# Kernel tuning notes

Measured on AMD Instinct MI355X. Metric: run time of the kernel, lower is better.

The kernel has to match this reference:

```python
import jax, jax.numpy as jnp
import numpy as np

B, N, D, H = 4, 256, 32, 512

def setup_inputs() -> dict:
    key = jax.random.key(0)
    ks = jax.random.split(key, 6)
    z = jax.random.normal(ks[0], (B, N, D), dtype=jnp.float32)
    motif_mask = (jax.random.uniform(ks[1], (B, N)) > 0.5).astype(jnp.float32)
    residue_mask = jnp.ones((B, N), dtype=jnp.float32)
    # Linear weights stored as (in, out); scaled like torch default init
    W1 = jax.random.normal(ks[2], (D * D, H), dtype=jnp.float32) / np.sqrt(D * D)
    b1 = jnp.zeros((H,), dtype=jnp.float32)
    W2 = jax.random.normal(ks[3], (H, H // 2), dtype=jnp.float32) / np.sqrt(H)
    b2 = jnp.zeros((H // 2,), dtype=jnp.float32)
    W3 = jax.random.normal(ks[4], (H // 2, 1), dtype=jnp.float32) / np.sqrt(H // 2)
    b3 = jnp.zeros((1,), dtype=jnp.float32)
    return {"z": z, "motif_mask": motif_mask, "residue_mask": residue_mask,
            "W1": W1, "b1": b1, "W2": W2, "b2": b2, "W3": W3, "b3": b3}

def reference(z, motif_mask, residue_mask, W1, b1, W2, b2, W3, b3):
    # kron[b,i,j, a*D+c] = z[b,i,a] * z[b,j,c]; first Linear on kron is the
    # bilinear form z_i^T W1_h z_j -- compute via two matmuls, never
    # materializing the (B,N,N,D^2) tensor.
    d = z.shape[-1]
    W1r = W1.reshape(d, d, -1)                      # (D, D, H); axis0 = z_i dim, axis1 = z_j dim
    tmp = jnp.einsum('bia,ach->bihc', z, W1r)        # (B, N, H, D)
    h1 = jax.nn.relu(jnp.einsum('bihc,bjc->bijh', tmp, z) + b1)  # (B, N, N, H)
    h2 = jax.nn.relu(jnp.einsum('bijh,hk->bijk', h1, W2) + b2)   # (B, N, N, H/2)
    contact_logits = (jnp.einsum('bijk,ko->bijo', h2, W3) + b3)[..., 0]  # (B, N, N)
    outer_mask = motif_mask[:, None, :] * motif_mask[:, :, None]
    contact_logits = contact_logits * outer_mask
    contact_map = jax.nn.sigmoid(contact_logits)
    return (contact_map, contact_logits)
```

## Files before the change

### kernel.cpp

```cpp
#include <hip/hip_runtime.h>
#include <hip/hip_bf16.h>
#include <cstdint>
#include <cstddef>

#define NB 4
#define NN 256
#define DD 32
#define HH 512

typedef __attribute__((ext_vector_type(8))) short short8;
typedef __attribute__((ext_vector_type(4))) float f32x4;
typedef __attribute__((ext_vector_type(16))) float f32x16;

static __device__ __forceinline__ unsigned cvtpk(float a, float b) {
  unsigned r;
  asm("v_cvt_pk_bf16_f32 %0, %1, %2" : "=v"(r) : "v"(a), "v"(b));
  return r;
}
static __device__ __forceinline__ unsigned short f2bf1(float a) {
  return (unsigned short)(cvtpk(a, 0.f) & 0xffffu);
}

static __device__ __forceinline__ short8 pack8(float4 a0, float4 a1) {
  union { unsigned u[4]; short8 s; } r;
  r.u[0] = cvtpk(a0.x, a0.y); r.u[1] = cvtpk(a0.z, a0.w);
  r.u[2] = cvtpk(a1.x, a1.y); r.u[3] = cvtpk(a1.z, a1.w);
  return r.s;
}

__global__ __launch_bounds__(256) void prep(const float* __restrict__ z,
                                            const float* __restrict__ W1,
                                            const float* __restrict__ W2,
                                            const float* __restrict__ motif,
                                            unsigned short* __restrict__ W2F,
                                            unsigned short* __restrict__ Tall,
                                            int* __restrict__ jlist,
                                            int* __restrict__ mlist,
                                            int* __restrict__ jcnt) {
  const int blk = blockIdx.x;
  const int tid = threadIdx.x;
  if (blk < 512) {
    __shared__ unsigned short w1s[16384];
    const int nblk = blk >> 4, mgrp = blk & 15;
    const int bibase = mgrp * 64;

    #pragma unroll
    for (int r = 0; r < 16; ++r) {
      int task = r * 256 + tid;
      int row = task >> 2;
      int hq = task & 3;
      float4 v = *(const float4*)(W1 + (size_t)row * 512 + nblk * 16 + hq * 4);
      int a = row >> 5, c = row & 31;
      int quad = a >> 3, e = a & 7;
      float hv[4] = {v.x, v.y, v.z, v.w};
      #pragma unroll
      for (int vv = 0; vv < 4; ++vv) {
        int hl = hq * 4 + vv;
        int nl = hl * 32 + c;
        int w2 = nl >> 7, r7 = nl & 127;
        int l16 = r7 >> 3, nt = r7 & 7;
        w1s[((w2 * 8 + nt) * 64 + quad * 16 + l16) * 8 + e] = f2bf1(hv[vv]);
      }
    }
    __syncthreads();

    const int w2 = tid >> 6, lane = tid & 63;
    const int quad = lane >> 4, l16 = lane & 15;

    short8 bfr[8];
    #pragma unroll
    for (int nt = 0; nt < 8; ++nt)
      bfr[nt] = *(const short8*)&w1s[((w2 * 8 + nt) * 64 + lane) * 8];

    const int ncol = nblk * 512 + w2 * 128 + l16 * 8;
    #pragma unroll
    for (int mtg = 0; mtg < 2; ++mtg) {
      short8 afr[2];
      #pragma unroll
      for (int mi = 0; mi < 2; ++mi) {
        const float* zr = z + (size_t)(bibase + (mtg * 2 + mi) * 16 + l16) * 32 + quad * 8;
        float4 a0 = *(const float4*)(zr);
        float4 a1 = *(const float4*)(zr + 4);
        afr[mi] = pack8(a0, a1);
      }
      f32x4 d[2][8];
      #pragma unroll
      for (int mi = 0; mi < 2; ++mi)
        #pragma unroll
        for (int nt = 0; nt < 8; ++nt)
          d[mi][nt] = __builtin_amdgcn_mfma_f32_16x16x32_bf16(
              afr[mi], bfr[nt], (f32x4){0.f, 0.f, 0.f, 0.f}, 0, 0, 0);
      #pragma unroll
      for (int mi = 0; mi < 2; ++mi)
        #pragma unroll
        for (int r = 0; r < 4; ++r) {
          size_t rowoff = (size_t)(bibase + (mtg * 2 + mi) * 16 + quad * 4 + r) * 16384;
          uint4 p;
          p.x = cvtpk(d[mi][0][r], d[mi][1][r]);
          p.y = cvtpk(d[mi][2][r], d[mi][3][r]);
          p.z = cvtpk(d[mi][4][r], d[mi][5][r]);
          p.w = cvtpk(d[mi][6][r], d[mi][7][r]);
          *(uint4*)&Tall[rowoff + ncol] = p;
        }
    }
  } else if (blk < 576) {
    int f8 = (blk - 512) * 256 + tid;
    int lane = f8 & 63;
    int nt = (f8 >> 6) & 1, s = (f8 >> 7) & 3, hc = (f8 >> 9) & 7, w = (f8 >> 12) & 3;
    int k2 = w * 64 + nt * 32 + (lane & 31);
    int hb = hc * 64 + s * 16 + (lane >> 5) * 8;
    float v[8];
    #pragma unroll
    for (int e = 0; e < 8; ++e) v[e] = W2[(hb + e) * 256 + k2];
    uint4 p;
    p.x = cvtpk(v[0], v[1]); p.y = cvtpk(v[2], v[3]);
    p.z = cvtpk(v[4], v[5]); p.w = cvtpk(v[6], v[7]);
    ((uint4*)W2F)[f8] = p;
  } else {
    const int w = tid >> 6, lane = tid & 63;
    if (w < NB) {
      int cnt = 0, mcnt = 0;
      #pragma unroll
      for (int ch = 0; ch < 4; ++ch) {
        int j = ch * 64 + lane;
        float m = motif[w * 256 + j];
        bool alive = (m != 0.f);
        unsigned long long mk = __ballot(alive);
        unsigned long long below = mk & ((1ull << lane) - 1ull);
        int pos = __popcll(below);
        if (alive) jlist[w * 256 + cnt + pos] = j;
        else       mlist[w * 256 + mcnt + (lane - pos)] = j;
        int pc = __popcll(mk);
        cnt += pc; mcnt += 64 - pc;
      }
      if (lane == 0) jcnt[w] = cnt;
    }
  }
}

__global__ __launch_bounds__(256) void fused(const unsigned short* __restrict__ Tall,
                                             const unsigned short* __restrict__ W2F,
                                             const float* __restrict__ z,
                                             const float* __restrict__ b1,
                                             const float* __restrict__ b2,
                                             const float* __restrict__ W3,
                                             const float* __restrict__ b3,
                                             const float* __restrict__ motif,
                                             const int* __restrict__ jlist,
                                             const int* __restrict__ mlist,
                                             const int* __restrict__ jcnt,
                                             float* __restrict__ out) {
  __shared__ unsigned short h1s[64 * 264];
  __shared__ float red[256];

  const int tid = threadIdx.x;
  const int w = tid >> 6, lane = tid & 63;
  const int quad = lane >> 4, l16 = lane & 15;
  const int L = lane >> 5, c32 = lane & 31;

  const int bx = blockIdx.x;
  const int jt = (bx >> 3) & 3;
  const int bi = (bx & 7) | ((bx >> 5) << 3);
  const int b = bi >> 8;
  const size_t OUT2 = (size_t)NB * NN * NN;

  const float mi_v = motif[bi];
  if (mi_v == 0.f) {
    if (tid < 64) {
      size_t idx = (size_t)bi * 256 + jt * 64 + tid;
      out[idx] = 0.5f;
      out[OUT2 + idx] = 0.f;
    }
    return;
  }

  const int cnt = jcnt[b];
  if (jt == 0) {
    int mcnt = 256 - cnt;
    if (tid < mcnt) {
      int jm = mlist[b * 256 + tid] & 255;
      size_t idx = (size_t)bi * 256 + jm;
      out[idx] = 0.5f;
      out[OUT2 + idx] = 0.f;
    }
  }
  if (jt * 64 >= cnt) return;
  const int slotbase = jt * 64;

  short8 zfr[4];
  #pragma unroll
  for (int nt = 0; nt < 4; ++nt) {
    int slot = slotbase + nt * 16 + l16;
    int sc = slot < cnt ? slot : cnt - 1;
    int jj = jlist[b * 256 + sc] & 255;
    const float* zr = z + (size_t)(b * 256 + jj) * 32 + quad * 8;
    float4 a0 = *(const float4*)(zr);
    float4 a1 = *(const float4*)(zr + 4);
    zfr[nt] = pack8(a0, a1);
  }

  float b2v[2], w3v[2];
  #pragma unroll
  for (int nt = 0; nt < 2; ++nt) {
    int k2 = w * 64 + nt * 32 + c32;
    b2v[nt] = b2[k2];
    w3v[nt] = W3[k2];
  }

  f32x16 acc[2][2];
  #pragma unroll
  for (int mt = 0; mt < 2; ++mt)
    #pragma unroll
    for (int nt = 0; nt < 2; ++nt)
      acc[mt][nt] = (f32x16){0.f,0.f,0.f,0.f,0.f,0.f,0.f,0.f,
                             0.f,0.f,0.f,0.f,0.f,0.f,0.f,0.f};

  const unsigned short* Tbase = Tall + (size_t)bi * 16384 + (w * 16 + l16) * 32 + quad * 8;
  const unsigned short* Wp = W2F + w * 32768 + lane * 8;
  const float* b1base = b1 + w * 16 + quad * 4;

  #pragma unroll
  for (int half = 0; half < 2; ++half) {
    short8 tfr[4];
    #pragma unroll
    for (int q = 0; q < 4; ++q)
      tfr[q] = *(const short8*)(Tbase + (half * 4 + q) * 2048);
    #pragma unroll
    for (int q = 0; q < 4; ++q) {
      float4 b1f = *(const float4*)(b1base + (half * 4 + q) * 64);
      f32x4 cin = {b1f.x, b1f.y, b1f.z, b1f.w};
      #pragma unroll
      for (int nt = 0; nt < 4; ++nt) {
        f32x4 d = __builtin_amdgcn_mfma_f32_16x16x32_bf16(tfr[q], zfr[nt], cin, 0, 0, 0);
        uint2 p;
        p.x = cvtpk(fmaxf(d[0], 0.f), fmaxf(d[1], 0.f));
        p.y = cvtpk(fmaxf(d[2], 0.f), fmaxf(d[3], 0.f));
        *(uint2*)&h1s[(nt * 16 + l16) * 264 + q * 64 + w * 16 + quad * 4] = p;
      }
    }
    __syncthreads();

    const unsigned short* Wh = Wp + half * 16384;
    const unsigned short* h1r = &h1s[c32 * 264 + L * 8];
    short8 bfp[3][2], afp[2][2];
    #pragma unroll
    for (int p = 0; p < 3; ++p) {
      bfp[p][0] = *(const short8*)(Wh + p * 1024);
      bfp[p][1] = *(const short8*)(Wh + p * 1024 + 512);
    }
    afp[0][0] = *(const short8*)(h1r);
    afp[0][1] = *(const short8*)(h1r + 32 * 264);
    afp[1][0] = *(const short8*)(h1r + 16);
    afp[1][1] = *(const short8*)(h1r + 32 * 264 + 16);
    #pragma unroll
    for (int u = 0; u < 16; ++u) {
      const int cur = u & 1, bq = u % 3;
      short8 a0 = afp[cur][0], a1 = afp[cur][1];
      short8 b0 = bfp[bq][0], b1q = bfp[bq][1];
      if (u < 14) {
        afp[cur][0] = *(const short8*)(h1r + (u + 2) * 16);
        afp[cur][1] = *(const short8*)(h1r + 32 * 264 + (u + 2) * 16);
      }
      if (u < 13) {
        bfp[bq][0] = *(const short8*)(Wh + (u + 3) * 1024);
        bfp[bq][1] = *(const short8*)(Wh + (u + 3) * 1024 + 512);
      }
      acc[0][0] = __builtin_amdgcn_mfma_f32_32x32x16_bf16(a0, b0, acc[0][0], 0, 0, 0);
      acc[0][1] = __builtin_amdgcn_mfma_f32_32x32x16_bf16(a0, b1q, acc[0][1], 0, 0, 0);
      acc[1][0] = __builtin_amdgcn_mfma_f32_32x32x16_bf16(a1, b0, acc[1][0], 0, 0, 0);
      acc[1][1] = __builtin_amdgcn_mfma_f32_32x32x16_bf16(a1, b1q, acc[1][1], 0, 0, 0);
    }
    if (half == 0) __syncthreads();
  }

  float pr[2][16];
  #pragma unroll
  for (int mt = 0; mt < 2; ++mt)
    #pragma unroll
    for (int reg = 0; reg < 16; ++reg) {
      float s = 0.f;
      #pragma unroll
      for (int nt = 0; nt < 2; ++nt) {
        float v = acc[mt][nt][reg] + b2v[nt];
        v = v > 0.f ? v : 0.f;
        s += v * w3v[nt];
      }
      s += __shfl_xor(s, 1);
      s += __shfl_xor(s, 2);
      s += __shfl_xor(s, 4);
      s += __shfl_xor(s, 8);
      s += __shfl_xor(s, 16);
      pr[mt][reg] = s;
    }
  if (c32 == 0) {
    #pragma unroll
    for (int mt = 0; mt < 2; ++mt)
      #pragma unroll
      for (int g = 0; g < 4; ++g) {
        float4 vv = {pr[mt][g * 4 + 0], pr[mt][g * 4 + 1],
                     pr[mt][g * 4 + 2], pr[mt][g * 4 + 3]};
        *(float4*)&red[w * 64 + mt * 32 + g * 8 + L * 4] = vv;
      }
  }
  __syncthreads();
  if (tid < 64) {
    int slot = slotbase + tid;
    if (slot < cnt) {
      int j = jlist[b * 256 + slot] & 255;
      float logit = red[tid] + red[64 + tid] + red[128 + tid] + red[192 + tid] + b3[0];
      float mm = mi_v * motif[b * 256 + j];
      logit *= mm;
      float map = 1.f / (1.f + expf(-logit));
      size_t idx = (size_t)bi * 256 + j;
      out[idx] = map;
      out[OUT2 + idx] = logit;
    }
  }
}

extern "C" void kernel_launch(void* const* d_in, const int* in_sizes, int n_in,
                              void* d_out, int out_size, void* d_ws, size_t ws_size,
                              hipStream_t stream) {
  const float* z     = (const float*)d_in[0];
  const float* motif = (const float*)d_in[1];
  const float* W1 = (const float*)d_in[3];
  const float* b1 = (const float*)d_in[4];
  const float* W2 = (const float*)d_in[5];
  const float* b2 = (const float*)d_in[6];
  const float* W3 = (const float*)d_in[7];
  const float* b3 = (const float*)d_in[8];
  float* out = (float*)d_out;

  char* ws = (char*)d_ws;
  unsigned short* Tall = (unsigned short*)ws;
  unsigned short* W2F  = (unsigned short*)(ws + 33554432);
  int* jlist = (int*)(ws + 33554432 + 262144);
  int* mlist = (int*)(ws + 33554432 + 262144 + 4096);
  int* jcnt  = (int*)(ws + 33554432 + 262144 + 8192);

  prep<<<577, 256, 0, stream>>>(z, W1, W2, motif, W2F, Tall, jlist, mlist, jcnt);
  fused<<<4096, 256, 0, stream>>>(Tall, W2F, z, b1, b2, W3, b3, motif,
                                  jlist, mlist, jcnt, out);
}
```

Before: 143.5 us.

## Use persistent blocks pulling compacted work items from an atomic queue

The prep kernel now builds a compact queue of (row, j-tile) items covering only live motif rows and needed j-tiles, and writes the masked outputs (0.5 and 0) in extra prep blocks. The fused kernel launches a fixed 1024 persistent blocks that fetch items through a global atomic counter, so it no longer launches 4096 blocks, most of which exit early. This cuts launch and early-exit overhead and balances load. In exchange it adds a per-item atomic, extra barriers, and a serial queue-building step in a single prep block.

New measurement: 161.0 us. 1.12x slower.

```diff
diff --git a/kernel.cpp b/kernel.cpp
--- a/kernel.cpp
+++ b/kernel.cpp
@@ -35,8 +35,11 @@
                                             unsigned short* __restrict__ W2F,
                                             unsigned short* __restrict__ Tall,
                                             int* __restrict__ jlist,
-                                            int* __restrict__ mlist,
-                                            int* __restrict__ jcnt) {
+                                            int* __restrict__ jcnt,
+                                            int* __restrict__ wq,
+                                            int* __restrict__ wqn,
+                                            int* __restrict__ ctr,
+                                            float* __restrict__ out) {
   const int blk = blockIdx.x;
   const int tid = threadIdx.x;
   if (blk < 512) {
@@ -116,10 +119,12 @@
     p.x = cvtpk(v[0], v[1]); p.y = cvtpk(v[2], v[3]);
     p.z = cvtpk(v[4], v[5]); p.w = cvtpk(v[6], v[7]);
     ((uint4*)W2F)[f8] = p;
-  } else {
+  } else if (blk == 576) {
+    __shared__ int itemc[4];
+    __shared__ int baseh[4];
     const int w = tid >> 6, lane = tid & 63;
+    int cnt = 0;
     if (w < NB) {
-      int cnt = 0, mcnt = 0;
       #pragma unroll
       for (int ch = 0; ch < 4; ++ch) {
         int j = ch * 64 + lane;
@@ -129,11 +134,51 @@
         unsigned long long below = mk & ((1ull << lane) - 1ull);
         int pos = __popcll(below);
         if (alive) jlist[w * 256 + cnt + pos] = j;
-        else       mlist[w * 256 + mcnt + (lane - pos)] = j;
-        int pc = __popcll(mk);
-        cnt += pc; mcnt += 64 - pc;
-      }
-      if (lane == 0) jcnt[w] = cnt;
+        cnt += __popcll(mk);
+      }
+      if (lane == 0) {
+        jcnt[w] = cnt;
+        itemc[w] = cnt * ((cnt + 63) >> 6);
+      }
+    }
+    __syncthreads();
+    if (tid == 0) {
+      int s = 0;
+      #pragma unroll
+      for (int k = 0; k < NB; ++k) { baseh[k] = s; s += itemc[k]; }
+      *wqn = s;
+      *ctr = 0;
+    }
+    __syncthreads();
+    if (w < NB) {
+      const int K = (cnt + 63) >> 6;
+      const int base = baseh[w];
+      int rank = 0;
+      #pragma unroll
+      for (int ch = 0; ch < 4; ++ch) {
+        int i = ch * 64 + lane;
+        bool alive = (motif[w * 256 + i] != 0.f);
+        unsigned long long mk = __ballot(alive);
+        unsigned long long below = mk & ((1ull << lane) - 1ull);
+        int pos = __popcll(below);
+        if (alive)
+          for (int jt = 0; jt < K; ++jt)
+            wq[base + (rank + pos) * K + jt] = (w * 256 + i) * 4 + jt;
+        rank += __popcll(mk);
+      }
+    }
+  } else {
+    const size_t OUT2 = (size_t)NB * NN * NN;
+    int t0 = (blk - 577) * 256 + tid;
+    #pragma unroll
+    for (int k = 0; k < 4; ++k) {
+      int p = t0 + k * 65536;
+      int bi = p >> 8, j = p & 255, b = bi >> 8;
+      bool masked = (motif[bi] == 0.f) || (motif[b * 256 + j] == 0.f);
+      if (masked) {
+        out[p] = 0.5f;
+        out[OUT2 + p] = 0.f;
+      }
     }
   }
 }
@@ -147,57 +192,21 @@
                                              const float* __restrict__ b3,
                                              const float* __restrict__ motif,
                                              const int* __restrict__ jlist,
-                                             const int* __restrict__ mlist,
                                              const int* __restrict__ jcnt,
+                                             const int* __restrict__ wq,
+                                             const int* __restrict__ wqn,
+                                             int* __restrict__ ctr,
                                              float* __restrict__ out) {
   __shared__ unsigned short h1s[64 * 264];
   __shared__ float red[256];
+  __shared__ int item_s;
 
   const int tid = threadIdx.x;
   const int w = tid >> 6, lane = tid & 63;
   const int quad = lane >> 4, l16 = lane & 15;
   const int L = lane >> 5, c32 = lane & 31;
-
-  const int bx = blockIdx.x;
-  const int jt = (bx >> 3) & 3;
-  const int bi = (bx & 7) | ((bx >> 5) << 3);
-  const int b = bi >> 8;
   const size_t OUT2 = (size_t)NB * NN * NN;
-
-  const float mi_v = motif[bi];
-  if (mi_v == 0.f) {
-    if (tid < 64) {
-      size_t idx = (size_t)bi * 256 + jt * 64 + tid;
-      out[idx] = 0.5f;
-      out[OUT2 + idx] = 0.f;
-    }
-    return;
-  }
-
-  const int cnt = jcnt[b];
-  if (jt == 0) {
-    int mcnt = 256 - cnt;
-    if (tid < mcnt) {
-      int jm = mlist[b * 256 + tid] & 255;
-      size_t idx = (size_t)bi * 256 + jm;
-      out[idx] = 0.5f;
-      out[OUT2 + idx] = 0.f;
-    }
-  }
-  if (jt * 64 >= cnt) return;
-  const int slotbase = jt * 64;
-
-  short8 zfr[4];
-  #pragma unroll
-  for (int nt = 0; nt < 4; ++nt) {
-    int slot = slotbase + nt * 16 + l16;
-    int sc = slot < cnt ? slot : cnt - 1;
-    int jj = jlist[b * 256 + sc] & 255;
-    const float* zr = z + (size_t)(b * 256 + jj) * 32 + quad * 8;
-    float4 a0 = *(const float4*)(zr);
-    float4 a1 = *(const float4*)(zr + 4);
-    zfr[nt] = pack8(a0, a1);
-  }
+  const int nitems = *wqn;
 
   float b2v[2], w3v[2];
   #pragma unroll
@@ -206,115 +215,141 @@
     b2v[nt] = b2[k2];
     w3v[nt] = W3[k2];
   }
-
-  f32x16 acc[2][2];
-  #pragma unroll
-  for (int mt = 0; mt < 2; ++mt)
-    #pragma unroll
-    for (int nt = 0; nt < 2; ++nt)
-      acc[mt][nt] = (f32x16){0.f,0.f,0.f,0.f,0.f,0.f,0.f,0.f,
-                             0.f,0.f,0.f,0.f,0.f,0.f,0.f,0.f};
-
-  const unsigned short* Tbase = Tall + (size_t)bi * 16384 + (w * 16 + l16) * 32 + quad * 8;
   const unsigned short* Wp = W2F + w * 32768 + lane * 8;
   const float* b1base = b1 + w * 16 + quad * 4;
 
-  #pragma unroll
-  for (int half = 0; half < 2; ++half) {
-    short8 tfr[4];
-    #pragma unroll
-    for (int q = 0; q < 4; ++q)
-      tfr[q] = *(const short8*)(Tbase + (half * 4 + q) * 2048);
-    #pragma unroll
-    for (int q = 0; q < 4; ++q) {
-      float4 b1f = *(const float4*)(b1base + (half * 4 + q) * 64);
-      f32x4 cin = {b1f.x, b1f.y, b1f.z, b1f.w};
-      #pragma unroll
-      for (int nt = 0; nt < 4; ++nt) {
-        f32x4 d = __builtin_amdgcn_mfma_f32_16x16x32_bf16(tfr[q], zfr[nt], cin, 0, 0, 0);
-        uint2 p;
-        p.x = cvtpk(fmaxf(d[0], 0.f), fmaxf(d[1], 0.f));
-        p.y = cvtpk(fmaxf(d[2], 0.f), fmaxf(d[3], 0.f));
-        *(uint2*)&h1s[(nt * 16 + l16) * 264 + q * 64 + w * 16 + quad * 4] = p;
-      }
-    }
-    __syncthreads();
-
-    const unsigned short* Wh = Wp + half * 16384;
-    const unsigned short* h1r = &h1s[c32 * 264 + L * 8];
-    short8 bfp[3][2], afp[2][2];
-    #pragma unroll
-    for (int p = 0; p < 3; ++p) {
-      bfp[p][0] = *(const short8*)(Wh + p * 1024);
-      bfp[p][1] = *(const short8*)(Wh + p * 1024 + 512);
-    }
-    afp[0][0] = *(const short8*)(h1r);
-    afp[0][1] = *(const short8*)(h1r + 32 * 264);
-    afp[1][0] = *(const short8*)(h1r + 16);
-    afp[1][1] = *(const short8*)(h1r + 32 * 264 + 16);
-    #pragma unroll
-    for (int u = 0; u < 16; ++u) {
-      const int cur = u & 1, bq = u % 3;
-      short8 a0 = afp[cur][0], a1 = afp[cur][1];
-      short8 b0 = bfp[bq][0], b1q = bfp[bq][1];
-      if (u < 14) {
-        afp[cur][0] = *(const short8*)(h1r + (u + 2) * 16);
-        afp[cur][1] = *(const short8*)(h1r + 32 * 264 + (u + 2) * 16);
-      }
-      if (u < 13) {
-        bfp[bq][0] = *(const short8*)(Wh + (u + 3) * 1024);
-        bfp[bq][1] = *(const short8*)(Wh + (u + 3) * 1024 + 512);
-      }
-      acc[0][0] = __builtin_amdgcn_mfma_f32_32x32x16_bf16(a0, b0, acc[0][0], 0, 0, 0);
-      acc[0][1] = __builtin_amdgcn_mfma_f32_32x32x16_bf16(a0, b1q, acc[0][1], 0, 0, 0);
-      acc[1][0] = __builtin_amdgcn_mfma_f32_32x32x16_bf16(a1, b0, acc[1][0], 0, 0, 0);
-      acc[1][1] = __builtin_amdgcn_mfma_f32_32x32x16_bf16(a1, b1q, acc[1][1], 0, 0, 0);
-    }
-    if (half == 0) __syncthreads();
-  }
-
-  float pr[2][16];
-  #pragma unroll
-  for (int mt = 0; mt < 2; ++mt)
-    #pragma unroll
-    for (int reg = 0; reg < 16; ++reg) {
-      float s = 0.f;
-      #pragma unroll
-      for (int nt = 0; nt < 2; ++nt) {
-        float v = acc[mt][nt][reg] + b2v[nt];
-        v = v > 0.f ? v : 0.f;
-        s += v * w3v[nt];
-      }
-      s += __shfl_xor(s, 1);
-      s += __shfl_xor(s, 2);
-      s += __shfl_xor(s, 4);
-      s += __shfl_xor(s, 8);
-      s += __shfl_xor(s, 16);
-      pr[mt][reg] = s;
-    }
-  if (c32 == 0) {
+  for (;;) {
+    if (tid == 0) item_s = atomicAdd(ctr, 1);
+    __syncthreads();
+    const int it = item_s;
+    if (it >= nitems) return;
+    const int item = wq[it];
+    const int bi = item >> 2, jt = item & 3;
+    const int b = bi >> 8;
+    const int cnt = jcnt[b];
+    const int slotbase = jt * 64;
+    const float mi_v = motif[bi];
+
+    short8 zfr[4];
+    #pragma unroll
+    for (int nt = 0; nt < 4; ++nt) {
+      int slot = slotbase + nt * 16 + l16;
+      int sc = slot < cnt ? slot : cnt - 1;
+      int jj = jlist[b * 256 + sc] & 255;
+      const float* zr = z + (size_t)(b * 256 + jj) * 32 + quad * 8;
+      float4 a0 = *(const float4*)(zr);
+      float4 a1 = *(const float4*)(zr + 4);
+      zfr[nt] = pack8(a0, a1);
+    }
+
+    f32x16 acc[2][2];
     #pragma unroll
     for (int mt = 0; mt < 2; ++mt)
       #pragma unroll
-      for (int g = 0; g < 4; ++g) {
-        float4 vv = {pr[mt][g * 4 + 0], pr[mt][g * 4 + 1],
-                     pr[mt][g * 4 + 2], pr[mt][g * 4 + 3]};
-        *(float4*)&red[w * 64 + mt * 32 + g * 8 + L * 4] = vv;
-      }
-  }
-  __syncthreads();
-  if (tid < 64) {
-    int slot = slotbase + tid;
-    if (slot < cnt) {
-      int j = jlist[b * 256 + slot] & 255;
-      float logit = red[tid] + red[64 + tid] + red[128 + tid] + red[192 + tid] + b3[0];
-      float mm = mi_v * motif[b * 256 + j];
-      logit *= mm;
-      float map = 1.f / (1.f + expf(-logit));
-      size_t idx = (size_t)bi * 256 + j;
-      out[idx] = map;
-      out[OUT2 + idx] = logit;
-    }
+      for (int nt = 0; nt < 2; ++nt)
+        acc[mt][nt] = (f32x16){0.f,0.f,0.f,0.f,0.f,0.f,0.f,0.f,
+                               0.f,0.f,0.f,0.f,0.f,0.f,0.f,0.f};
+
+    const unsigned short* Tbase = Tall + (size_t)bi * 16384 + (w * 16 + l16) * 32 + quad * 8;
+
+    #pragma unroll
+    for (int half = 0; half < 2; ++half) {
+      short8 tfr[4];
+      #pragma unroll
+      for (int q = 0; q < 4; ++q)
+        tfr[q] = *(const short8*)(Tbase + (half * 4 + q) * 2048);
+      #pragma unroll
+      for (int q = 0; q < 4; ++q) {
+        float4 b1f = *(const float4*)(b1base + (half * 4 + q) * 64);
+        f32x4 cin = {b1f.x, b1f.y, b1f.z, b1f.w};
+        #pragma unroll
+        for (int nt = 0; nt < 4; ++nt) {
+          f32x4 d = __builtin_amdgcn_mfma_f32_16x16x32_bf16(tfr[q], zfr[nt], cin, 0, 0, 0);
+          uint2 p;
+          p.x = cvtpk(fmaxf(d[0], 0.f), fmaxf(d[1], 0.f));
+          p.y = cvtpk(fmaxf(d[2], 0.f), fmaxf(d[3], 0.f));
+          *(uint2*)&h1s[(nt * 16 + l16) * 264 + q * 64 + w * 16 + quad * 4] = p;
+        }
+      }
+      __syncthreads();
+
+      const unsigned short* Wh = Wp + half * 16384;
+      const unsigned short* h1r = &h1s[c32 * 264 + L * 8];
+      short8 bfp[3][2], afp[2][2];
+      #pragma unroll
+      for (int p = 0; p < 3; ++p) {
+        bfp[p][0] = *(const short8*)(Wh + p * 1024);
+        bfp[p][1] = *(const short8*)(Wh + p * 1024 + 512);
+      }
+      afp[0][0] = *(const short8*)(h1r);
+      afp[0][1] = *(const short8*)(h1r + 32 * 264);
+      afp[1][0] = *(const short8*)(h1r + 16);
+      afp[1][1] = *(const short8*)(h1r + 32 * 264 + 16);
+      #pragma unroll
+      for (int u = 0; u < 16; ++u) {
+        const int cur = u & 1, bq = u % 3;
+        short8 a0 = afp[cur][0], a1 = afp[cur][1];
+        short8 b0 = bfp[bq][0], b1q = bfp[bq][1];
+        if (u < 14) {
+          afp[cur][0] = *(const short8*)(h1r + (u + 2) * 16);
+          afp[cur][1] = *(const short8*)(h1r + 32 * 264 + (u + 2) * 16);
+        }
+        if (u < 13) {
+          bfp[bq][0] = *(const short8*)(Wh + (u + 3) * 1024);
+          bfp[bq][1] = *(const short8*)(Wh + (u + 3) * 1024 + 512);
+        }
+        acc[0][0] = __builtin_amdgcn_mfma_f32_32x32x16_bf16(a0, b0, acc[0][0], 0, 0, 0);
+        acc[0][1] = __builtin_amdgcn_mfma_f32_32x32x16_bf16(a0, b1q, acc[0][1], 0, 0, 0);
+        acc[1][0] = __builtin_amdgcn_mfma_f32_32x32x16_bf16(a1, b0, acc[1][0], 0, 0, 0);
+        acc[1][1] = __builtin_amdgcn_mfma_f32_32x32x16_bf16(a1, b1q, acc[1][1], 0, 0, 0);
+      }
+      __syncthreads();
+    }
+
+    float pr[2][16];
+    #pragma unroll
+    for (int mt = 0; mt < 2; ++mt)
+      #pragma unroll
+      for (int reg = 0; reg < 16; ++reg) {
+        float s = 0.f;
+        #pragma unroll
+        for (int nt = 0; nt < 2; ++nt) {
+          float v = acc[mt][nt][reg] + b2v[nt];
+          v = v > 0.f ? v : 0.f;
+          s += v * w3v[nt];
+        }
+        s += __shfl_xor(s, 1);
+        s += __shfl_xor(s, 2);
+        s += __shfl_xor(s, 4);
+        s += __shfl_xor(s, 8);
+        s += __shfl_xor(s, 16);
+        pr[mt][reg] = s;
+      }
+    if (c32 == 0) {
+      #pragma unroll
+      for (int mt = 0; mt < 2; ++mt)
+        #pragma unroll
+        for (int g = 0; g < 4; ++g) {
+          float4 vv = {pr[mt][g * 4 + 0], pr[mt][g * 4 + 1],
+                       pr[mt][g * 4 + 2], pr[mt][g * 4 + 3]};
+          *(float4*)&red[w * 64 + mt * 32 + g * 8 + L * 4] = vv;
+        }
+    }
+    __syncthreads();
+    if (tid < 64) {
+      int slot = slotbase + tid;
+      if (slot < cnt) {
+        int j = jlist[b * 256 + slot] & 255;
+        float logit = red[tid] + red[64 + tid] + red[128 + tid] + red[192 + tid] + b3[0];
+        float mm = mi_v * motif[b * 256 + j];
+        logit *= mm;
+        float map = 1.f / (1.f + expf(-logit));
+        size_t idx = (size_t)bi * 256 + j;
+        out[idx] = map;
+        out[OUT2 + idx] = logit;
+      }
+    }
+    __syncthreads();
   }
 }
 
@@ -335,10 +370,13 @@
   unsigned short* Tall = (unsigned short*)ws;
   unsigned short* W2F  = (unsigned short*)(ws + 33554432);
   int* jlist = (int*)(ws + 33554432 + 262144);
-  int* mlist = (int*)(ws + 33554432 + 262144 + 4096);
-  int* jcnt  = (int*)(ws + 33554432 + 262144 + 8192);
-
-  prep<<<577, 256, 0, stream>>>(z, W1, W2, motif, W2F, Tall, jlist, mlist, jcnt);
-  fused<<<4096, 256, 0, stream>>>(Tall, W2F, z, b1, b2, W3, b3, motif,
-                                  jlist, mlist, jcnt, out);
-}
+  int* jcnt  = (int*)(ws + 33554432 + 262144 + 4096);
+  int* wq    = (int*)(ws + 33554432 + 262144 + 4096 + 64);
+  int* wqn   = (int*)(ws + 33554432 + 262144 + 4096 + 64 + 16384);
+  int* ctr   = (int*)(ws + 33554432 + 262144 + 4096 + 64 + 16384 + 64);
+
+  prep<<<833, 256, 0, stream>>>(z, W1, W2, motif, W2F, Tall,
+                                jlist, jcnt, wq, wqn, ctr, out);
+  fused<<<1024, 256, 0, stream>>>(Tall, W2F, z, b1, b2, W3, b3, motif,
+                                  jlist, jcnt, wq, wqn, ctr, out);
+}
```
